# Kernel optimization log

Hardware: AMD Instinct MI355X
Metric: run time of the kernel (lower is better)

The kernel has to match this reference:

```python
import jax, jax.numpy as jnp
import numpy as np

B, T, D = 4, 2048, 1024
NUM_HEADS = 16
HEAD_DIM = D // NUM_HEADS
MLP_HIDDEN = int(D * 4.0)  # 4096; gate_proj -> 2*MLP_HIDDEN
LN_EPS = 1e-6
GN_EPS = 1e-5


def rmsnorm(x, eps=1e-8):
    return x * jax.lax.rsqrt(jnp.mean(x * x, axis=-1, keepdims=True) + eps)


def bitlinear(x, w):
    # mmfreelm BitLinear: RMSNorm -> 8-bit per-token act quant (STE) -> ternary weight quant (STE)
    xn = rmsnorm(x)
    s = 127.0 / jnp.clip(jnp.max(jnp.abs(xn), axis=-1, keepdims=True), 1e-5, None)
    xq = xn + jax.lax.stop_gradient(jnp.clip(jnp.round(xn * s), -128, 127) / s - xn)
    ws = 1.0 / jnp.clip(jnp.mean(jnp.abs(w)), 1e-5, None)
    wq = w + jax.lax.stop_gradient(jnp.clip(jnp.round(w * ws), -1, 1) / ws - w)
    return xq @ wq.T


def layernorm(x, eps=LN_EPS):  # non-affine
    mu = jnp.mean(x, axis=-1, keepdims=True)
    var = jnp.mean((x - mu) ** 2, axis=-1, keepdims=True)
    return (x - mu) * jax.lax.rsqrt(var + eps)


def modulate(x, shift, scale):
    return x * (1.0 + scale[:, None, :]) + shift[:, None, :]


def hgrn_attention(x, wi, wf, wg, gnorm_w, wo):
    i = bitlinear(x, wi)
    f = jax.nn.sigmoid(bitlinear(x, wf))
    i = jax.nn.silu(i) * (1.0 - f)  # swiglu(i, 1-f)
    # gated linear recurrence h_t = f_t * h_{t-1} + i_t along time axis
    def combine(c1, c2):
        a1, b1 = c1
        a2, b2 = c2
        return a1 * a2, b1 * a2 + b2
    _, h = jax.lax.associative_scan(combine, (f, i), axis=1)
    g = bitlinear(x, wg)
    hh = h.reshape(B, T, NUM_HEADS, HEAD_DIM)
    gg = g.reshape(B, T, NUM_HEADS, HEAD_DIM)
    # FusedRMSNormSwishGate over head_dim
    o = rmsnorm(hh, GN_EPS) * gnorm_w * (gg * jax.nn.sigmoid(gg))
    return bitlinear(o.reshape(B, T, D), wo)


def hgrn_mlp(x, gate_w, down_w):
    y = bitlinear(x, gate_w)
    gate, y = jnp.split(y, 2, axis=-1)
    return bitlinear(jax.nn.silu(gate) * y, down_w)


def setup_inputs() -> dict:
    key = jax.random.key(0)
    ks = jax.random.split(key, 16)
    p = lambda k, shape: jax.random.normal(k, shape, dtype=jnp.float32) * 0.02
    return {
        "x": jax.random.normal(ks[0], (B, T, D), dtype=jnp.float32),
        "c": jax.random.normal(ks[1], (B, D), dtype=jnp.float32),
        "adaln_w": p(ks[2], (6 * D, D)),
        "adaln_b": jnp.zeros((6 * D,), dtype=jnp.float32),
        "wi": p(ks[3], (D, D)),
        "wf": p(ks[4], (D, D)),
        "wg": p(ks[5], (D, D)),
        "gnorm_w": jnp.ones((HEAD_DIM,), dtype=jnp.float32),
        "wo": p(ks[6], (D, D)),
        "gate_w": p(ks[7], (2 * MLP_HIDDEN, D)),
        "down_w": p(ks[8], (D, MLP_HIDDEN)),
    }


def reference(x, c, adaln_w, adaln_b, wi, wf, wg, gnorm_w, wo, gate_w, down_w):
    params = jax.nn.silu(c) @ adaln_w.T + adaln_b  # [B, 6D]
    (shift_msa, scale_msa, gate_msa,
     shift_mlp, scale_mlp, gate_mlp) = jnp.split(params, 6, axis=1)
    mod_x = modulate(layernorm(x), shift_msa, scale_msa)
    attn_out = hgrn_attention(mod_x, wi, wf, wg, gnorm_w, wo)
    x = x + gate_msa[:, None, :] * attn_out
    mlp_in = modulate(layernorm(x), shift_mlp, scale_mlp)
    x = x + gate_mlp[:, None, :] * hgrn_mlp(mlp_in, gate_w, down_w)
    return x
```

## Files before the change

kernel.cpp:

```cpp
#include <hip/hip_runtime.h>
#include <cstdint>
#include <cstddef>

#define B_   4
#define T_   2048
#define D_   1024
#define NTOK (B_*T_)
#define HID  4096
#define PDIM (6*D_)

typedef int v4i __attribute__((ext_vector_type(4)));
typedef __attribute__((ext_vector_type(8))) unsigned short ushort8v;

__device__ __forceinline__ float sigf(float x){ return 1.0f/(1.0f+expf(-x)); }

__device__ __forceinline__ float b2f(uint16_t u){ union{uint32_t i; float f;} x; x.i = ((uint32_t)u)<<16; return x.f; }
__device__ __forceinline__ uint16_t f2b(float f){
  union{float f; uint32_t i;} x; x.f=f;
  uint32_t r = x.i + 0x7fff + ((x.i>>16)&1);
  return (uint16_t)(r>>16);
}

__device__ __forceinline__ int swz_word(int wi, int row){
  return (wi & ~15) | ((((wi>>2)&3) ^ ((row>>1)&3))<<2) | (wi&3);
}

__device__ __forceinline__ float bsum256(float v, float* sm, int tid){
#pragma unroll
  for (int o=32;o;o>>=1) v += __shfl_down(v,o);
  if ((tid&63)==0) sm[tid>>6]=v;
  __syncthreads();
  float r = sm[0]+sm[1]+sm[2]+sm[3];
  __syncthreads();
  return r;
}
__device__ __forceinline__ void bsummax256(float& s, float& m, float* sm, int tid){
#pragma unroll
  for (int o=32;o;o>>=1){ s += __shfl_down(s,o); m = fmaxf(m,__shfl_down(m,o)); }
  if ((tid&63)==0){ sm[tid>>6]=s; sm[4+(tid>>6)]=m; }
  __syncthreads();
  s = sm[0]+sm[1]+sm[2]+sm[3];
  m = fmaxf(fmaxf(sm[4],sm[5]),fmaxf(sm[6],sm[7]));
  __syncthreads();
}

__device__ __forceinline__ uint32_t pack4(float a, float b, float c, float d, float k){
  int q0=(int)rintf(a*k); q0 = q0<-128?-128:(q0>127?127:q0);
  int q1=(int)rintf(b*k); q1 = q1<-128?-128:(q1>127?127:q1);
  int q2=(int)rintf(c*k); q2 = q2<-128?-128:(q2>127?127:q2);
  int q3=(int)rintf(d*k); q3 = q3<-128?-128:(q3>127?127:q3);
  return (uint32_t)(q0&255) | ((uint32_t)(q1&255)<<8) | ((uint32_t)(q2&255)<<16) | ((uint32_t)(q3&255)<<24);
}

struct WMeta {
  const float* w[6];
  int8_t* q[6];
  int n[6];
  int kws[6];
};

__global__ __launch_bounds__(256) void k_wabs(WMeta meta, float* __restrict__ partial){
  int mat = blockIdx.y;
  const float* w = meta.w[mat];
  int n = meta.n[mat];
  int tid = threadIdx.x;
  float s = 0.f;
  for (int i = blockIdx.x*256 + tid; i < n; i += 256*gridDim.x) s += fabsf(w[i]);
  __shared__ float sm[4];
#pragma unroll
  for (int o=32;o;o>>=1) s += __shfl_down(s,o);
  if ((tid&63)==0) sm[tid>>6]=s;
  __syncthreads();
  if (tid==0) partial[mat*256 + blockIdx.x] = sm[0]+sm[1]+sm[2]+sm[3];
}

__global__ __launch_bounds__(256) void k_wfin(WMeta meta, const float* __restrict__ partial, float* __restrict__ wdeq){
  int mat = blockIdx.x;
  int tid = threadIdx.x;
  float s = partial[mat*256 + tid];
  __shared__ float sm[4];
#pragma unroll
  for (int o=32;o;o>>=1) s += __shfl_down(s,o);
  if ((tid&63)==0) sm[tid>>6]=s;
  __syncthreads();
  if (tid==0){
    float mean = (sm[0]+sm[1]+sm[2]+sm[3]) / (float)meta.n[mat];
    wdeq[mat] = fmaxf(mean, 1e-5f);
  }
}

__global__ __launch_bounds__(256) void k_wquant(WMeta meta, const float* __restrict__ wdeq){
  int mat = blockIdx.y;
  const float* w = meta.w[mat];
  uint32_t* q = (uint32_t*)meta.q[mat];
  int nw = meta.n[mat]>>2;
  int kws = meta.kws[mat];
  int kwmask = (1<<kws)-1;
  float ws = 1.0f / wdeq[mat];
  for (int i = blockIdx.x*256 + threadIdx.x; i < nw; i += 256*gridDim.x){
    float4 v = ((const float4*)w)[i];
    int q0=(int)rintf(v.x*ws); q0=q0<-1?-1:(q0>1?1:q0);
    int q1=(int)rintf(v.y*ws); q1=q1<-1?-1:(q1>1?1:q1);
    int q2=(int)rintf(v.z*ws); q2=q2<-1?-1:(q2>1?1:q2);
    int q3=(int)rintf(v.w*ws); q3=q3<-1?-1:(q3>1?1:q3);
    uint32_t packed = (uint32_t)(q0&255) | ((uint32_t)(q1&255)<<8) | ((uint32_t)(q2&255)<<16) | ((uint32_t)(q3&255)<<24);
    int row = i >> kws, wi = i & kwmask;
    q[((size_t)row<<kws) + swz_word(wi,row)] = packed;
  }
}

__global__ __launch_bounds__(256) void k_adaln(const float* __restrict__ c, const float* __restrict__ w,
                                               const float* __restrict__ bias, float* __restrict__ params){
  int wv = threadIdx.x>>6, lane = threadIdx.x&63;
  int oidx = blockIdx.x*4 + wv;
  int b = oidx / PDIM, j = oidx % PDIM;
  const float* cr = c + b*D_;
  const float* wr = w + (size_t)j*D_;
  float s = 0.f;
  for (int k = lane; k < D_; k += 64){
    float cv = cr[k];
    s += (cv*sigf(cv)) * wr[k];
  }
#pragma unroll
  for (int o=32;o;o>>=1) s += __shfl_down(s,o);
  if (lane==0) params[oidx] = s + bias[j];
}

template<int RES>
__global__ __launch_bounds__(256) void k_lnmodq(const float* __restrict__ xin,
    const float* __restrict__ addv, const float* __restrict__ params,
    int shift_off, int scale_off, int gate_off,
    float* __restrict__ x2out, int8_t* __restrict__ xq, float* __restrict__ dq){
  int tok = blockIdx.x;
  int b = tok >> 11;
  int tid = threadIdx.x;
  __shared__ float sm[8];
  const float* pb = params + (size_t)b*PDIM;
  float4 v = ((const float4*)(xin + (size_t)tok*D_))[tid];
  if (RES){
    float4 a = ((const float4*)(addv + (size_t)tok*D_))[tid];
    float4 g = ((const float4*)(pb + gate_off))[tid];
    v.x = fmaf(g.x,a.x,v.x); v.y = fmaf(g.y,a.y,v.y);
    v.z = fmaf(g.z,a.z,v.z); v.w = fmaf(g.w,a.w,v.w);
    ((float4*)(x2out + (size_t)tok*D_))[tid] = v;
  }
  float mu = bsum256(v.x+v.y+v.z+v.w, sm, tid) * (1.0f/D_);
  float t0=v.x-mu, t1=v.y-mu, t2=v.z-mu, t3=v.w-mu;
  float var = bsum256(t0*t0+t1*t1+t2*t2+t3*t3, sm, tid) * (1.0f/D_);
  float rstd = rsqrtf(var + 1e-6f);
  float4 sc = ((const float4*)(pb + scale_off))[tid];
  float4 sh = ((const float4*)(pb + shift_off))[tid];
  float y0 = fmaf(t0*rstd, 1.0f+sc.x, sh.x);
  float y1 = fmaf(t1*rstd, 1.0f+sc.y, sh.y);
  float y2 = fmaf(t2*rstd, 1.0f+sc.z, sh.z);
  float y3 = fmaf(t3*rstd, 1.0f+sc.w, sh.w);
  float ssq = y0*y0+y1*y1+y2*y2+y3*y3;
  float mx = fmaxf(fmaxf(fabsf(y0),fabsf(y1)),fmaxf(fabsf(y2),fabsf(y3)));
  bsummax256(ssq, mx, sm, tid);
  float rms = rsqrtf(ssq*(1.0f/D_) + 1e-8f);
  float a = fmaxf(mx*rms, 1e-5f);
  float s = 127.0f/a;
  float k = rms*s;
  ((uint32_t*)(xq + (size_t)tok*D_))[swz_word(tid,tok)] = pack4(y0,y1,y2,y3,k);
  if (tid==0) dq[tok] = 1.0f/s;
}

template<int MODE>
__global__ __launch_bounds__(256) void k_gemm(const int8_t* __restrict__ Aq, const int8_t* __restrict__ Bq,
    void* __restrict__ Outv, const float* __restrict__ adq, const float* __restrict__ wdq_ptr,
    int N, int K, const float* __restrict__ resid, const float* __restrict__ params){
  __shared__ int8_t lA[2][8192], lB[2][8192];
  const int tid = threadIdx.x;
  const int wave = tid>>6, lane = tid&63;
  const int row0 = blockIdx.y<<7, col0 = blockIdx.x<<7;
  const int wm = (wave>>1)<<6, wn = (wave&1)<<6;
  v4i acc[4][4];
#pragma unroll
  for (int m=0;m<4;m++)
#pragma unroll
    for (int n=0;n<4;n++) acc[m][n] = (v4i){0,0,0,0};
  const int rA = lane&15, kg = lane>>4;
  const int axor = (rA>>1)&3;
  const int r_st = tid>>2, cb_st = (tid&3)<<4;

  auto STAGE = [&](int buf, int k0){
#pragma unroll
    for (int p=0;p<2;p++){
      int r = p*64 + r_st;
      __builtin_amdgcn_global_load_lds((const __attribute__((address_space(1))) void*)(Aq + (size_t)(row0+r)*K + k0 + cb_st),
        (__attribute__((address_space(3))) void*)(&lA[buf][p*4096 + wave*1024]), 16, 0, 0);
      __builtin_amdgcn_global_load_lds((const __attribute__((address_space(1))) void*)(Bq + (size_t)(col0+r)*K + k0 + cb_st),
        (__attribute__((address_space(3))) void*)(&lB[buf][p*4096 + wave*1024]), 16, 0, 0);
    }
  };
  auto COMPUTE = [&](int buf){
    const v4i* la4 = (const v4i*)lA[buf];
    const v4i* lb4 = (const v4i*)lB[buf];
    v4i af[4], bf[4];
#pragma unroll
    for (int m=0;m<4;m++){ int r = wm + m*16 + rA; af[m] = la4[(r<<2) + (kg^axor)]; }
#pragma unroll
    for (int n=0;n<4;n++){ int r = wn + n*16 + rA; bf[n] = lb4[(r<<2) + (kg^axor)]; }
#pragma unroll
    for (int m=0;m<4;m++)
#pragma unroll
      for (int n=0;n<4;n++)
        acc[m][n] = __builtin_amdgcn_mfma_i32_16x16x64_i8(af[m], bf[n], acc[m][n], 0, 0, 0);
  };

  STAGE(0, 0);
  __syncthreads();
  int cur = 0;
  for (int k0=64; k0<K; k0+=64){
    STAGE(cur^1, k0);
    COMPUTE(cur);
    __syncthreads();
    cur ^= 1;
  }
  COMPUTE(cur);

  float wdq = wdq_ptr[0];
  int rr = (lane>>4)<<2, cl = lane&15;
#pragma unroll
  for (int m=0;m<4;m++){
#pragma unroll
    for (int r=0;r<4;r++){
      int row = row0 + wm + m*16 + rr + r;
      float scale = adq[row]*wdq;
#pragma unroll
      for (int n=0;n<4;n++){
        int col = col0 + wn + n*16 + cl;
        size_t oi = (size_t)row*N + col;
        float val = (float)acc[m][n][r]*scale;
        if (MODE==0) ((float*)Outv)[oi] = val;
        if (MODE==1) ((uint16_t*)Outv)[oi] = f2b(val);
        if (MODE==2){
          int bb = row>>11;
          ((float*)Outv)[oi] = resid[oi] + params[(size_t)bb*PDIM + 5*D_ + col]*val;
        }
      }
    }
  }
}

template<int MODE>
__global__ __launch_bounds__(256) void k_gemm2(const int8_t* __restrict__ Aq, const int8_t* __restrict__ Bq0,
    const int8_t* __restrict__ Bq1, uint16_t* __restrict__ out0, uint16_t* __restrict__ out1,
    const float* __restrict__ adq, const float* __restrict__ wdq_ptr, int i0, int i1, int N, int K){
  __shared__ int8_t lA[2][8192], lB0[2][8192], lB1[2][8192];
  const int tid = threadIdx.x;
  const int wave = tid>>6, lane = tid&63;
  const int row0 = blockIdx.y<<7, col0 = blockIdx.x<<7;
  const int wm = (wave>>1)<<6, wn = (wave&1)<<6;
  v4i acc0[4][4], acc1[4][4];
#pragma unroll
  for (int m=0;m<4;m++)
#pragma unroll
    for (int n=0;n<4;n++){ acc0[m][n] = (v4i){0,0,0,0}; acc1[m][n] = (v4i){0,0,0,0}; }
  const int rA = lane&15, kg = lane>>4;
  const int axor = (rA>>1)&3;
  const int r_st = tid>>2, cb_st = (tid&3)<<4;

  auto STAGE = [&](int buf, int k0){
#pragma unroll
    for (int p=0;p<2;p++){
      int r = p*64 + r_st;
      __builtin_amdgcn_global_load_lds((const __attribute__((address_space(1))) void*)(Aq  + (size_t)(row0+r)*K + k0 + cb_st),
        (__attribute__((address_space(3))) void*)(&lA[buf][p*4096 + wave*1024]), 16, 0, 0);
      __builtin_amdgcn_global_load_lds((const __attribute__((address_space(1))) void*)(Bq0 + (size_t)(col0+r)*K + k0 + cb_st),
        (__attribute__((address_space(3))) void*)(&lB0[buf][p*4096 + wave*1024]), 16, 0, 0);
      __builtin_amdgcn_global_load_lds((const __attribute__((address_space(1))) void*)(Bq1 + (size_t)(col0+r)*K + k0 + cb_st),
        (__attribute__((address_space(3))) void*)(&lB1[buf][p*4096 + wave*1024]), 16, 0, 0);
    }
  };
  auto COMPUTE = [&](int buf){
    const v4i* la4 = (const v4i*)lA[buf];
    const v4i* lb4 = (const v4i*)lB0[buf];
    const v4i* lc4 = (const v4i*)lB1[buf];
    v4i af[4], bf[4], cf[4];
#pragma unroll
    for (int m=0;m<4;m++){ int r = wm + m*16 + rA; af[m] = la4[(r<<2) + (kg^axor)]; }
#pragma unroll
    for (int n=0;n<4;n++){ int r = wn + n*16 + rA; bf[n] = lb4[(r<<2) + (kg^axor)]; cf[n] = lc4[(r<<2) + (kg^axor)]; }
#pragma unroll
    for (int m=0;m<4;m++)
#pragma unroll
      for (int n=0;n<4;n++){
        acc0[m][n] = __builtin_amdgcn_mfma_i32_16x16x64_i8(af[m], bf[n], acc0[m][n], 0, 0, 0);
        acc1[m][n] = __builtin_amdgcn_mfma_i32_16x16x64_i8(af[m], cf[n], acc1[m][n], 0, 0, 0);
      }
  };

  STAGE(0, 0);
  __syncthreads();
  int cur = 0;
  for (int k0=64; k0<K; k0+=64){
    STAGE(cur^1, k0);
    COMPUTE(cur);
    __syncthreads();
    cur ^= 1;
  }
  COMPUTE(cur);

  float wdq0 = wdq_ptr[i0], wdq1 = wdq_ptr[i1];
  int rr = (lane>>4)<<2, cl = lane&15;
#pragma unroll
  for (int m=0;m<4;m++){
#pragma unroll
    for (int r=0;r<4;r++){
      int row = row0 + wm + m*16 + rr + r;
      float scale = adq[row];
#pragma unroll
      for (int n=0;n<4;n++){
        int col = col0 + wn + n*16 + cl;
        size_t oi = (size_t)row*N + col;
        float v0 = (float)acc0[m][n][r]*scale*wdq0;
        float v1 = (float)acc1[m][n][r]*scale*wdq1;
        if (MODE==0){
          float fs = sigf(v1);
          out0[oi] = f2b(v0*sigf(v0)*(1.0f-fs));
          out1[oi] = f2b(fs);
        } else {
          out0[oi] = f2b(v0*sigf(v0)*v1);
        }
      }
    }
  }
}

__global__ __launch_bounds__(256) void k_scanA(const uint16_t* __restrict__ f, const uint16_t* __restrict__ ii,
                                               float* __restrict__ Ac, float* __restrict__ Hc){
  int idx = blockIdx.x*256 + threadIdx.x;
  int ch = idx >> 12;
  int c  = idx & 4095;
  int b = c >> 10, d = c & 1023;
  size_t base = ((size_t)(b*T_ + ch*64))*D_ + d;
  float a = 1.f, h = 0.f;
  for (int t=0;t<64;t++){
    float ft = b2f(f[base + (size_t)t*D_]);
    float it = b2f(ii[base + (size_t)t*D_]);
    a *= ft;
    h = ft*h + it;
  }
  Ac[ch*4096 + c] = a;
  Hc[ch*4096 + c] = h;
}
__global__ __launch_bounds__(256) void k_scanB(const float* __restrict__ Ac, const float* __restrict__ Hc,
                                               float* __restrict__ H0){
  int c = blockIdx.x*256 + threadIdx.x;
  float h = 0.f;
  for (int ch=0; ch<32; ch++){
    H0[ch*4096 + c] = h;
    h = Ac[ch*4096 + c]*h + Hc[ch*4096 + c];
  }
}
__global__ __launch_bounds__(256) void k_scanC(const uint16_t* __restrict__ f, const uint16_t* __restrict__ ii,
                                               const float* __restrict__ H0, float* __restrict__ hout){
  int idx = blockIdx.x*256 + threadIdx.x;
  int ch = idx >> 12;
  int c  = idx & 4095;
  int b = c >> 10, d = c & 1023;
  size_t base = ((size_t)(b*T_ + ch*64))*D_ + d;
  float h = H0[ch*4096 + c];
  for (int t=0;t<64;t++){
    float ft = b2f(f[base + (size_t)t*D_]);
    float it = b2f(ii[base + (size_t)t*D_]);
    h = ft*h + it;
    hout[base + (size_t)t*D_] = h;
  }
}

__global__ __launch_bounds__(256) void k_ogateq(const float* __restrict__ h, const uint16_t* __restrict__ g,
    const float* __restrict__ gnw, int8_t* __restrict__ xq, float* __restrict__ dq){
  int tok = blockIdx.x, tid = threadIdx.x;
  __shared__ float sm[8];
  float4 hv = ((const float4*)(h + (size_t)tok*D_))[tid];
  float ss = hv.x*hv.x + hv.y*hv.y + hv.z*hv.z + hv.w*hv.w;
  ss += __shfl_xor(ss,1); ss += __shfl_xor(ss,2); ss += __shfl_xor(ss,4); ss += __shfl_xor(ss,8);
  float rh = rsqrtf(ss*(1.0f/64.0f) + 1e-5f);
  ushort4 gv = ((const ushort4*)(g + (size_t)tok*D_))[tid];
  float g0=b2f(gv.x), g1=b2f(gv.y), g2=b2f(gv.z), g3=b2f(gv.w);
  int hd = (tid*4)&63;
  float o0 = hv.x*rh*gnw[hd+0]*(g0*sigf(g0));
  float o1 = hv.y*rh*gnw[hd+1]*(g1*sigf(g1));
  float o2 = hv.z*rh*gnw[hd+2]*(g2*sigf(g2));
  float o3 = hv.w*rh*gnw[hd+3]*(g3*sigf(g3));
  float ssq = o0*o0+o1*o1+o2*o2+o3*o3;
  float mx = fmaxf(fmaxf(fabsf(o0),fabsf(o1)),fmaxf(fabsf(o2),fabsf(o3)));
  bsummax256(ssq, mx, sm, tid);
  float rms = rsqrtf(ssq*(1.0f/D_) + 1e-8f);
  float a = fmaxf(mx*rms, 1e-5f);
  float s = 127.0f/a;
  float k = rms*s;
  ((uint32_t*)(xq + (size_t)tok*D_))[swz_word(tid,tok)] = pack4(o0,o1,o2,o3,k);
  if (tid==0) dq[tok] = 1.0f/s;
}

__global__ __launch_bounds__(256) void k_mlpq(const uint16_t* __restrict__ hsw, int8_t* __restrict__ xq,
                                              float* __restrict__ dq){
  int tok = blockIdx.x, tid = threadIdx.x;
  __shared__ float sm[8];
  const ushort8v* r8 = (const ushort8v*)(hsw + (size_t)tok*HID);
  float v[2][8];
  float ssq = 0.f, mx = 0.f;
#pragma unroll
  for (int j=0;j<2;j++){
    ushort8v u = r8[tid + j*256];
#pragma unroll
    for (int e=0;e<8;e++){
      float fv = b2f(u[e]);
      v[j][e] = fv;
      ssq += fv*fv;
      mx = fmaxf(mx, fabsf(fv));
    }
  }
  bsummax256(ssq, mx, sm, tid);
  float rms = rsqrtf(ssq*(1.0f/HID) + 1e-8f);
  float a = fmaxf(mx*rms, 1e-5f);
  float s = 127.0f/a;
  float k = rms*s;
  uint32_t* qw = (uint32_t*)(xq + (size_t)tok*HID);
#pragma unroll
  for (int j=0;j<2;j++){
    int u = tid + j*256;
    qw[swz_word(2*u,   tok)] = pack4(v[j][0],v[j][1],v[j][2],v[j][3],k);
    qw[swz_word(2*u+1, tok)] = pack4(v[j][4],v[j][5],v[j][6],v[j][7],k);
  }
  if (tid==0) dq[tok] = 1.0f/s;
}


extern "C" void kernel_launch(void* const* d_in, const int* in_sizes, int n_in,
                              void* d_out, int out_size, void* d_ws, size_t ws_size,
                              hipStream_t stream){
  (void)in_sizes; (void)n_in; (void)out_size; (void)ws_size;
  const float* x     = (const float*)d_in[0];
  const float* c     = (const float*)d_in[1];
  const float* aw    = (const float*)d_in[2];
  const float* ab    = (const float*)d_in[3];
  const float* wi    = (const float*)d_in[4];
  const float* wf    = (const float*)d_in[5];
  const float* wg    = (const float*)d_in[6];
  const float* gnw   = (const float*)d_in[7];
  const float* wo    = (const float*)d_in[8];
  const float* wgate = (const float*)d_in[9];
  const float* wdown = (const float*)d_in[10];
  float* out = (float*)d_out;

  char* ws = (char*)d_ws;
  size_t off = 0;
  auto alloc = [&](size_t b){ size_t r = off; off += (b + 255) & ~(size_t)255; return r; };

  size_t oWQ[6];
  oWQ[0] = alloc(1024*1024);
  oWQ[1] = alloc(1024*1024);
  oWQ[2] = alloc(1024*1024);
  oWQ[3] = alloc(1024*1024);
  oWQ[4] = alloc((size_t)8192*1024);
  oWQ[5] = alloc((size_t)1024*4096);
  size_t oWDEQ = alloc(6*4);
  size_t oPART = alloc(6*256*4);
  size_t oPAR  = alloc((size_t)4*PDIM*4);
  size_t oS1 = alloc(NTOK*4), oS2 = alloc(NTOK*4), oS3 = alloc(NTOK*4), oSH = alloc(NTOK*4);
  size_t oXQA  = alloc((size_t)NTOK*D_);
  size_t oPOOL = alloc((size_t)3*NTOK*D_*2 + (size_t)2*NTOK*D_*4);
  size_t oX2   = alloc((size_t)NTOK*D_*4);
  size_t oSA = alloc((size_t)32*4096*4), oSHc = alloc((size_t)32*4096*4), oSH0 = alloc((size_t)32*4096*4);

  float*  params = (float*)(ws+oPAR);
  float*  wdeq   = (float*)(ws+oWDEQ);
  float*  part   = (float*)(ws+oPART);
  float*  s1 = (float*)(ws+oS1); float* s2 = (float*)(ws+oS2);
  float*  s3 = (float*)(ws+oS3); float* sh = (float*)(ws+oSH);
  int8_t* xqa = (int8_t*)(ws+oXQA);
  uint16_t* bI  = (uint16_t*)(ws+oPOOL);
  uint16_t* bF  = bI + (size_t)NTOK*D_;
  uint16_t* bG  = bF + (size_t)NTOK*D_;
  float*    bufH  = (float*)(bG + (size_t)NTOK*D_);
  float*    bufAT = bufH + (size_t)NTOK*D_;
  uint16_t* hsw   = bI;
  int8_t*   xqh   = (int8_t*)bufAT;
  float*  x2    = (float*)(ws+oX2);
  float*  scAc = (float*)(ws+oSA); float* scHc = (float*)(ws+oSHc); float* scH0 = (float*)(ws+oSH0);

  WMeta meta;
  meta.w[0]=wi; meta.w[1]=wf; meta.w[2]=wg; meta.w[3]=wo; meta.w[4]=wgate; meta.w[5]=wdown;
  for (int m=0;m<6;m++) meta.q[m] = (int8_t*)(ws+oWQ[m]);
  meta.n[0]=meta.n[1]=meta.n[2]=meta.n[3]=1024*1024; meta.n[4]=8192*1024; meta.n[5]=1024*4096;
  meta.kws[0]=meta.kws[1]=meta.kws[2]=meta.kws[3]=meta.kws[4]=8; meta.kws[5]=10;

  k_wabs  <<<dim3(256,6), 256, 0, stream>>>(meta, part);
  k_wfin  <<<6,           256, 0, stream>>>(meta, part, wdeq);
  k_wquant<<<dim3(1024,6),256, 0, stream>>>(meta, wdeq);

  k_adaln<<<PDIM, 256, 0, stream>>>(c, aw, ab, params);

  k_lnmodq<0><<<NTOK, 256, 0, stream>>>(x, nullptr, params, 0, D_, 0, nullptr, xqa, s1);
  k_gemm2<0><<<dim3(8,64), 256, 0, stream>>>(xqa, meta.q[0], meta.q[1], bI, bF, s1, wdeq, 0, 1, D_, D_);
  k_gemm<1><<<dim3(8,64), 256, 0, stream>>>(xqa, meta.q[2], bG, s1, wdeq+2, D_, D_, nullptr, nullptr);
  k_scanA<<<512, 256, 0, stream>>>(bF, bI, scAc, scHc);
  k_scanB<<<16,  256, 0, stream>>>(scAc, scHc, scH0);
  k_scanC<<<512, 256, 0, stream>>>(bF, bI, scH0, bufH);
  k_ogateq<<<NTOK, 256, 0, stream>>>(bufH, bG, gnw, xqa, s2);
  k_gemm<0><<<dim3(8,64), 256, 0, stream>>>(xqa, meta.q[3], bufAT, s2, wdeq+3, D_, D_, nullptr, nullptr);

  k_lnmodq<1><<<NTOK, 256, 0, stream>>>(x, bufAT, params, 3*D_, 4*D_, 2*D_, x2, xqa, s3);
  k_gemm2<1><<<dim3(32,64), 256, 0, stream>>>(xqa, meta.q[4], meta.q[4] + (size_t)HID*1024, hsw, nullptr, s3, wdeq+4, 0, 0, HID, D_);
  k_mlpq<<<NTOK, 256, 0, stream>>>(hsw, xqh, sh);
  k_gemm<2><<<dim3(8,64), 256, 0, stream>>>(xqh, meta.q[5], out, sh, wdeq+5, D_, HID, x2, params);
}
```

Before: 603.9 us.

## Triple-buffer GEMM pipelines, store intermediates in fp32, batch adaLN over four rows

```diff
diff --git a/kernel.cpp b/kernel.cpp
--- a/kernel.cpp
+++ b/kernel.cpp
@@ -10,16 +10,10 @@
 #define PDIM (6*D_)
 
 typedef int v4i __attribute__((ext_vector_type(4)));
-typedef __attribute__((ext_vector_type(8))) unsigned short ushort8v;
 
 __device__ __forceinline__ float sigf(float x){ return 1.0f/(1.0f+expf(-x)); }
 
-__device__ __forceinline__ float b2f(uint16_t u){ union{uint32_t i; float f;} x; x.i = ((uint32_t)u)<<16; return x.f; }
-__device__ __forceinline__ uint16_t f2b(float f){
-  union{float f; uint32_t i;} x; x.f=f;
-  uint32_t r = x.i + 0x7fff + ((x.i>>16)&1);
-  return (uint16_t)(r>>16);
-}
+#define VWAIT(n) asm volatile("s_waitcnt vmcnt(" #n ")" ::: "memory")
 
 __device__ __forceinline__ int swz_word(int wi, int row){
   return (wi & ~15) | ((((wi>>2)&3) ^ ((row>>1)&3))<<2) | (wi&3);
@@ -109,21 +103,43 @@
   }
 }
 
-__global__ __launch_bounds__(256) void k_adaln(const float* __restrict__ c, const float* __restrict__ w,
+__global__ __launch_bounds__(256) void k_siluc(const float* __restrict__ c, float* __restrict__ siluc){
+  int i = blockIdx.x*256 + threadIdx.x;
+  float v = c[i];
+  siluc[i] = v*sigf(v);
+}
+__global__ __launch_bounds__(256) void k_adaln(const float* __restrict__ siluc, const float* __restrict__ w,
                                                const float* __restrict__ bias, float* __restrict__ params){
   int wv = threadIdx.x>>6, lane = threadIdx.x&63;
-  int oidx = blockIdx.x*4 + wv;
-  int b = oidx / PDIM, j = oidx % PDIM;
-  const float* cr = c + b*D_;
-  const float* wr = w + (size_t)j*D_;
-  float s = 0.f;
-  for (int k = lane; k < D_; k += 64){
-    float cv = cr[k];
-    s += (cv*sigf(cv)) * wr[k];
-  }
-#pragma unroll
-  for (int o=32;o;o>>=1) s += __shfl_down(s,o);
-  if (lane==0) params[oidx] = s + bias[j];
+  int j = blockIdx.x*4 + wv;
+  const float4* wr = (const float4*)(w + (size_t)j*D_);
+  const float4* c0 = (const float4*)(siluc);
+  const float4* c1 = (const float4*)(siluc + 1024);
+  const float4* c2 = (const float4*)(siluc + 2048);
+  const float4* c3 = (const float4*)(siluc + 3072);
+  float s0=0.f, s1=0.f, s2=0.f, s3=0.f;
+#pragma unroll
+  for (int it=0; it<4; ++it){
+    int k4 = it*64 + lane;
+    float4 wk = wr[k4];
+    float4 a0 = c0[k4], a1 = c1[k4], a2 = c2[k4], a3 = c3[k4];
+    s0 += wk.x*a0.x + wk.y*a0.y + wk.z*a0.z + wk.w*a0.w;
+    s1 += wk.x*a1.x + wk.y*a1.y + wk.z*a1.z + wk.w*a1.w;
+    s2 += wk.x*a2.x + wk.y*a2.y + wk.z*a2.z + wk.w*a2.w;
+    s3 += wk.x*a3.x + wk.y*a3.y + wk.z*a3.z + wk.w*a3.w;
+  }
+#pragma unroll
+  for (int o=32;o;o>>=1){
+    s0 += __shfl_down(s0,o); s1 += __shfl_down(s1,o);
+    s2 += __shfl_down(s2,o); s3 += __shfl_down(s3,o);
+  }
+  if (lane==0){
+    float bj = bias[j];
+    params[j]          = s0 + bj;
+    params[PDIM + j]   = s1 + bj;
+    params[2*PDIM + j] = s2 + bj;
+    params[3*PDIM + j] = s3 + bj;
+  }
 }
 
 template<int RES>
@@ -167,9 +183,9 @@
 
 template<int MODE>
 __global__ __launch_bounds__(256) void k_gemm(const int8_t* __restrict__ Aq, const int8_t* __restrict__ Bq,
-    void* __restrict__ Outv, const float* __restrict__ adq, const float* __restrict__ wdq_ptr,
+    float* __restrict__ Out, const float* __restrict__ adq, const float* __restrict__ wdq_ptr,
     int N, int K, const float* __restrict__ resid, const float* __restrict__ params){
-  __shared__ int8_t lA[2][8192], lB[2][8192];
+  __shared__ int8_t lA[3][8192], lB[3][8192];
   const int tid = threadIdx.x;
   const int wave = tid>>6, lane = tid&63;
   const int row0 = blockIdx.y<<7, col0 = blockIdx.x<<7;
@@ -208,16 +224,32 @@
         acc[m][n] = __builtin_amdgcn_mfma_i32_16x16x64_i8(af[m], bf[n], acc[m][n], 0, 0, 0);
   };
 
+  const int nt = K>>6;
   STAGE(0, 0);
-  __syncthreads();
-  int cur = 0;
-  for (int k0=64; k0<K; k0+=64){
-    STAGE(cur^1, k0);
-    COMPUTE(cur);
-    __syncthreads();
-    cur ^= 1;
-  }
-  COMPUTE(cur);
+  STAGE(1, 64);
+  int bc = 0, k0 = 128;
+  for (int t=0; t<nt-2; ++t){
+    int bs = bc+2; if (bs>=3) bs-=3;
+    STAGE(bs, k0); k0 += 64;
+    VWAIT(8);
+    __builtin_amdgcn_sched_barrier(0);
+    __builtin_amdgcn_s_barrier();
+    __builtin_amdgcn_sched_barrier(0);
+    COMPUTE(bc);
+    __builtin_amdgcn_s_barrier();
+    if (++bc==3) bc=0;
+  }
+  VWAIT(4);
+  __builtin_amdgcn_sched_barrier(0);
+  __builtin_amdgcn_s_barrier();
+  __builtin_amdgcn_sched_barrier(0);
+  COMPUTE(bc);
+  if (++bc==3) bc=0;
+  VWAIT(0);
+  __builtin_amdgcn_sched_barrier(0);
+  __builtin_amdgcn_s_barrier();
+  __builtin_amdgcn_sched_barrier(0);
+  COMPUTE(bc);
 
   float wdq = wdq_ptr[0];
   int rr = (lane>>4)<<2, cl = lane&15;
@@ -232,12 +264,11 @@
         int col = col0 + wn + n*16 + cl;
         size_t oi = (size_t)row*N + col;
         float val = (float)acc[m][n][r]*scale;
-        if (MODE==0) ((float*)Outv)[oi] = val;
-        if (MODE==1) ((uint16_t*)Outv)[oi] = f2b(val);
         if (MODE==2){
           int bb = row>>11;
-          ((float*)Outv)[oi] = resid[oi] + params[(size_t)bb*PDIM + 5*D_ + col]*val;
+          val = resid[oi] + params[(size_t)bb*PDIM + 5*D_ + col]*val;
         }
+        Out[oi] = val;
       }
     }
   }
@@ -245,9 +276,9 @@
 
 template<int MODE>
 __global__ __launch_bounds__(256) void k_gemm2(const int8_t* __restrict__ Aq, const int8_t* __restrict__ Bq0,
-    const int8_t* __restrict__ Bq1, uint16_t* __restrict__ out0, uint16_t* __restrict__ out1,
+    const int8_t* __restrict__ Bq1, float* __restrict__ out0, float* __restrict__ out1,
     const float* __restrict__ adq, const float* __restrict__ wdq_ptr, int i0, int i1, int N, int K){
-  __shared__ int8_t lA[2][8192], lB0[2][8192], lB1[2][8192];
+  __shared__ int8_t lA[3][8192], lB0[3][8192], lB1[3][8192];
   const int tid = threadIdx.x;
   const int wave = tid>>6, lane = tid&63;
   const int row0 = blockIdx.y<<7, col0 = blockIdx.x<<7;
@@ -291,16 +322,32 @@
       }
   };
 
+  const int nt = K>>6;
   STAGE(0, 0);
-  __syncthreads();
-  int cur = 0;
-  for (int k0=64; k0<K; k0+=64){
-    STAGE(cur^1, k0);
-    COMPUTE(cur);
-    __syncthreads();
-    cur ^= 1;
-  }
-  COMPUTE(cur);
+  STAGE(1, 64);
+  int bc = 0, k0 = 128;
+  for (int t=0; t<nt-2; ++t){
+    int bs = bc+2; if (bs>=3) bs-=3;
+    STAGE(bs, k0); k0 += 64;
+    VWAIT(12);
+    __builtin_amdgcn_sched_barrier(0);
+    __builtin_amdgcn_s_barrier();
+    __builtin_amdgcn_sched_barrier(0);
+    COMPUTE(bc);
+    __builtin_amdgcn_s_barrier();
+    if (++bc==3) bc=0;
+  }
+  VWAIT(6);
+  __builtin_amdgcn_sched_barrier(0);
+  __builtin_amdgcn_s_barrier();
+  __builtin_amdgcn_sched_barrier(0);
+  COMPUTE(bc);
+  if (++bc==3) bc=0;
+  VWAIT(0);
+  __builtin_amdgcn_sched_barrier(0);
+  __builtin_amdgcn_s_barrier();
+  __builtin_amdgcn_sched_barrier(0);
+  COMPUTE(bc);
 
   float wdq0 = wdq_ptr[i0], wdq1 = wdq_ptr[i1];
   int rr = (lane>>4)<<2, cl = lane&15;
@@ -318,17 +365,17 @@
         float v1 = (float)acc1[m][n][r]*scale*wdq1;
         if (MODE==0){
           float fs = sigf(v1);
-          out0[oi] = f2b(v0*sigf(v0)*(1.0f-fs));
-          out1[oi] = f2b(fs);
+          out0[oi] = v0*sigf(v0)*(1.0f-fs);
+          out1[oi] = fs;
         } else {
-          out0[oi] = f2b(v0*sigf(v0)*v1);
+          out0[oi] = v0*sigf(v0)*v1;
         }
       }
     }
   }
 }
 
-__global__ __launch_bounds__(256) void k_scanA(const uint16_t* __restrict__ f, const uint16_t* __restrict__ ii,
+__global__ __launch_bounds__(256) void k_scanA(const float* __restrict__ f, const float* __restrict__ ii,
                                                float* __restrict__ Ac, float* __restrict__ Hc){
   int idx = blockIdx.x*256 + threadIdx.x;
   int ch = idx >> 12;
@@ -337,8 +384,8 @@
   size_t base = ((size_t)(b*T_ + ch*64))*D_ + d;
   float a = 1.f, h = 0.f;
   for (int t=0;t<64;t++){
-    float ft = b2f(f[base + (size_t)t*D_]);
-    float it = b2f(ii[base + (size_t)t*D_]);
+    float ft = f[base + (size_t)t*D_];
+    float it = ii[base + (size_t)t*D_];
     a *= ft;
     h = ft*h + it;
   }
@@ -354,7 +401,7 @@
     h = Ac[ch*4096 + c]*h + Hc[ch*4096 + c];
   }
 }
-__global__ __launch_bounds__(256) void k_scanC(const uint16_t* __restrict__ f, const uint16_t* __restrict__ ii,
+__global__ __launch_bounds__(256) void k_scanC(const float* __restrict__ f, const float* __restrict__ ii,
                                                const float* __restrict__ H0, float* __restrict__ hout){
   int idx = blockIdx.x*256 + threadIdx.x;
   int ch = idx >> 12;
@@ -363,14 +410,14 @@
   size_t base = ((size_t)(b*T_ + ch*64))*D_ + d;
   float h = H0[ch*4096 + c];
   for (int t=0;t<64;t++){
-    float ft = b2f(f[base + (size_t)t*D_]);
-    float it = b2f(ii[base + (size_t)t*D_]);
+    float ft = f[base + (size_t)t*D_];
+    float it = ii[base + (size_t)t*D_];
     h = ft*h + it;
     hout[base + (size_t)t*D_] = h;
   }
 }
 
-__global__ __launch_bounds__(256) void k_ogateq(const float* __restrict__ h, const uint16_t* __restrict__ g,
+__global__ __launch_bounds__(256) void k_ogateq(const float* __restrict__ h, const float* __restrict__ g,
     const float* __restrict__ gnw, int8_t* __restrict__ xq, float* __restrict__ dq){
   int tok = blockIdx.x, tid = threadIdx.x;
   __shared__ float sm[8];
@@ -378,13 +425,12 @@
   float ss = hv.x*hv.x + hv.y*hv.y + hv.z*hv.z + hv.w*hv.w;
   ss += __shfl_xor(ss,1); ss += __shfl_xor(ss,2); ss += __shfl_xor(ss,4); ss += __shfl_xor(ss,8);
   float rh = rsqrtf(ss*(1.0f/64.0f) + 1e-5f);
-  ushort4 gv = ((const ushort4*)(g + (size_t)tok*D_))[tid];
-  float g0=b2f(gv.x), g1=b2f(gv.y), g2=b2f(gv.z), g3=b2f(gv.w);
+  float4 gv = ((const float4*)(g + (size_t)tok*D_))[tid];
   int hd = (tid*4)&63;
-  float o0 = hv.x*rh*gnw[hd+0]*(g0*sigf(g0));
-  float o1 = hv.y*rh*gnw[hd+1]*(g1*sigf(g1));
-  float o2 = hv.z*rh*gnw[hd+2]*(g2*sigf(g2));
-  float o3 = hv.w*rh*gnw[hd+3]*(g3*sigf(g3));
+  float o0 = hv.x*rh*gnw[hd+0]*(gv.x*sigf(gv.x));
+  float o1 = hv.y*rh*gnw[hd+1]*(gv.y*sigf(gv.y));
+  float o2 = hv.z*rh*gnw[hd+2]*(gv.z*sigf(gv.z));
+  float o3 = hv.w*rh*gnw[hd+3]*(gv.w*sigf(gv.w));
   float ssq = o0*o0+o1*o1+o2*o2+o3*o3;
   float mx = fmaxf(fmaxf(fabsf(o0),fabsf(o1)),fmaxf(fabsf(o2),fabsf(o3)));
   bsummax256(ssq, mx, sm, tid);
@@ -396,23 +442,18 @@
   if (tid==0) dq[tok] = 1.0f/s;
 }
 
-__global__ __launch_bounds__(256) void k_mlpq(const uint16_t* __restrict__ hsw, int8_t* __restrict__ xq,
+__global__ __launch_bounds__(256) void k_mlpq(const float* __restrict__ hsw, int8_t* __restrict__ xq,
                                               float* __restrict__ dq){
   int tok = blockIdx.x, tid = threadIdx.x;
   __shared__ float sm[8];
-  const ushort8v* r8 = (const ushort8v*)(hsw + (size_t)tok*HID);
-  float v[2][8];
+  const float4* r4 = (const float4*)(hsw + (size_t)tok*HID);
+  float4 v[4];
   float ssq = 0.f, mx = 0.f;
 #pragma unroll
-  for (int j=0;j<2;j++){
-    ushort8v u = r8[tid + j*256];
-#pragma unroll
-    for (int e=0;e<8;e++){
-      float fv = b2f(u[e]);
-      v[j][e] = fv;
-      ssq += fv*fv;
-      mx = fmaxf(mx, fabsf(fv));
-    }
+  for (int j=0;j<4;j++){
+    v[j] = r4[tid + j*256];
+    ssq += v[j].x*v[j].x + v[j].y*v[j].y + v[j].z*v[j].z + v[j].w*v[j].w;
+    mx = fmaxf(mx, fmaxf(fmaxf(fabsf(v[j].x),fabsf(v[j].y)),fmaxf(fabsf(v[j].z),fabsf(v[j].w))));
   }
   bsummax256(ssq, mx, sm, tid);
   float rms = rsqrtf(ssq*(1.0f/HID) + 1e-8f);
@@ -421,11 +462,8 @@
   float k = rms*s;
   uint32_t* qw = (uint32_t*)(xq + (size_t)tok*HID);
 #pragma unroll
-  for (int j=0;j<2;j++){
-    int u = tid + j*256;
-    qw[swz_word(2*u,   tok)] = pack4(v[j][0],v[j][1],v[j][2],v[j][3],k);
-    qw[swz_word(2*u+1, tok)] = pack4(v[j][4],v[j][5],v[j][6],v[j][7],k);
-  }
+  for (int j=0;j<4;j++)
+    qw[swz_word(tid + j*256, tok)] = pack4(v[j].x,v[j].y,v[j].z,v[j].w,k);
   if (tid==0) dq[tok] = 1.0f/s;
 }
 
@@ -460,26 +498,28 @@
   oWQ[5] = alloc((size_t)1024*4096);
   size_t oWDEQ = alloc(6*4);
   size_t oPART = alloc(6*256*4);
+  size_t oSILC = alloc(4096*4);
   size_t oPAR  = alloc((size_t)4*PDIM*4);
   size_t oS1 = alloc(NTOK*4), oS2 = alloc(NTOK*4), oS3 = alloc(NTOK*4), oSH = alloc(NTOK*4);
   size_t oXQA  = alloc((size_t)NTOK*D_);
-  size_t oPOOL = alloc((size_t)3*NTOK*D_*2 + (size_t)2*NTOK*D_*4);
+  size_t oPOOL = alloc((size_t)5*NTOK*D_*4);
   size_t oX2   = alloc((size_t)NTOK*D_*4);
   size_t oSA = alloc((size_t)32*4096*4), oSHc = alloc((size_t)32*4096*4), oSH0 = alloc((size_t)32*4096*4);
 
   float*  params = (float*)(ws+oPAR);
   float*  wdeq   = (float*)(ws+oWDEQ);
   float*  part   = (float*)(ws+oPART);
+  float*  silc   = (float*)(ws+oSILC);
   float*  s1 = (float*)(ws+oS1); float* s2 = (float*)(ws+oS2);
   float*  s3 = (float*)(ws+oS3); float* sh = (float*)(ws+oSH);
   int8_t* xqa = (int8_t*)(ws+oXQA);
-  uint16_t* bI  = (uint16_t*)(ws+oPOOL);
-  uint16_t* bF  = bI + (size_t)NTOK*D_;
-  uint16_t* bG  = bF + (size_t)NTOK*D_;
-  float*    bufH  = (float*)(bG + (size_t)NTOK*D_);
-  float*    bufAT = bufH + (size_t)NTOK*D_;
-  uint16_t* hsw   = bI;
-  int8_t*   xqh   = (int8_t*)bufAT;
+  float*  bufI  = (float*)(ws+oPOOL);
+  float*  bufF  = bufI + (size_t)NTOK*D_;
+  float*  bufG  = bufF + (size_t)NTOK*D_;
+  float*  bufH  = bufG + (size_t)NTOK*D_;
+  float*  bufAT = bufH + (size_t)NTOK*D_;
+  float*  hsw   = bufI;
+  int8_t* xqh   = (int8_t*)bufAT;
   float*  x2    = (float*)(ws+oX2);
   float*  scAc = (float*)(ws+oSA); float* scHc = (float*)(ws+oSHc); float* scH0 = (float*)(ws+oSH0);
 
@@ -493,15 +533,16 @@
   k_wfin  <<<6,           256, 0, stream>>>(meta, part, wdeq);
   k_wquant<<<dim3(1024,6),256, 0, stream>>>(meta, wdeq);
 
-  k_adaln<<<PDIM, 256, 0, stream>>>(c, aw, ab, params);
+  k_siluc<<<16, 256, 0, stream>>>(c, silc);
+  k_adaln<<<PDIM/4, 256, 0, stream>>>(silc, aw, ab, params);
 
   k_lnmodq<0><<<NTOK, 256, 0, stream>>>(x, nullptr, params, 0, D_, 0, nullptr, xqa, s1);
-  k_gemm2<0><<<dim3(8,64), 256, 0, stream>>>(xqa, meta.q[0], meta.q[1], bI, bF, s1, wdeq, 0, 1, D_, D_);
-  k_gemm<1><<<dim3(8,64), 256, 0, stream>>>(xqa, meta.q[2], bG, s1, wdeq+2, D_, D_, nullptr, nullptr);
-  k_scanA<<<512, 256, 0, stream>>>(bF, bI, scAc, scHc);
+  k_gemm2<0><<<dim3(8,64), 256, 0, stream>>>(xqa, meta.q[0], meta.q[1], bufI, bufF, s1, wdeq, 0, 1, D_, D_);
+  k_gemm<0><<<dim3(8,64), 256, 0, stream>>>(xqa, meta.q[2], bufG, s1, wdeq+2, D_, D_, nullptr, nullptr);
+  k_scanA<<<512, 256, 0, stream>>>(bufF, bufI, scAc, scHc);
   k_scanB<<<16,  256, 0, stream>>>(scAc, scHc, scH0);
-  k_scanC<<<512, 256, 0, stream>>>(bF, bI, scH0, bufH);
-  k_ogateq<<<NTOK, 256, 0, stream>>>(bufH, bG, gnw, xqa, s2);
+  k_scanC<<<512, 256, 0, stream>>>(bufF, bufI, scH0, bufH);
+  k_ogateq<<<NTOK, 256, 0, stream>>>(bufH, bufG, gnw, xqa, s2);
   k_gemm<0><<<dim3(8,64), 256, 0, stream>>>(xqa, meta.q[3], bufAT, s2, wdeq+3, D_, D_, nullptr, nullptr);
 
   k_lnmodq<1><<<NTOK, 256, 0, stream>>>(x, bufAT, params, 3*D_, 4*D_, 2*D_, x2, xqa, s3);
```

Result: slower. 676.0 us (+11.9%).
